# Kernel optimization log

Measured on AMD Instinct MI355X. Metric: run time of the kernel, lower is better.

Reference implementation:

```python
import jax, jax.numpy as jnp
import numpy as np

H = 128

def _gru_cell(x, h, w_ih, w_hh, b_ih, b_hh):
    # PyTorch GRUCell semantics; w_* are [3H, H], gate order r, z, n.
    gi = x @ w_ih.T + b_ih
    gh = h @ w_hh.T + b_hh
    ir, iz, in_ = jnp.split(gi, 3, axis=-1)
    hr, hz, hn = jnp.split(gh, 3, axis=-1)
    r = jax.nn.sigmoid(ir + hr)
    z = jax.nn.sigmoid(iz + hz)
    n = jnp.tanh(in_ + r * hn)
    return (1.0 - z) * n + z * h


def setup_inputs() -> dict:
    key = jax.random.key(0)
    ks = jax.random.split(key, 24)
    s = 0.05
    d = {}
    d["weapon_features"] = jax.random.normal(ks[0], (4, 8, 64, 4), jnp.float32)
    d["target_features"] = jax.random.normal(ks[1], (4, 8, 64, 4), jnp.float32)
    d["edge_features"] = jax.random.uniform(ks[2], (4, 8, 64, 64, 1), jnp.float32)
    # projections (torch Linear convention: weight [out, in])
    d["wp_w"] = jax.random.normal(ks[3], (H, 4), jnp.float32) * s
    d["wp_b"] = jnp.zeros((H,), jnp.float32)
    d["tp_w"] = jax.random.normal(ks[4], (H, 4), jnp.float32) * s
    d["tp_b"] = jnp.zeros((H,), jnp.float32)
    d["ep_w"] = jax.random.normal(ks[5], (H, 1), jnp.float32) * s
    d["ep_b"] = jnp.zeros((H,), jnp.float32)
    # message / edge-update linears [H, 3H]
    d["eu_w"] = jax.random.normal(ks[6], (H, 3 * H), jnp.float32) * s
    d["eu_b"] = jnp.zeros((H,), jnp.float32)
    d["wm_w"] = jax.random.normal(ks[7], (H, 3 * H), jnp.float32) * s
    d["wm_b"] = jnp.zeros((H,), jnp.float32)
    d["tm_w"] = jax.random.normal(ks[8], (H, 3 * H), jnp.float32) * s
    d["tm_b"] = jnp.zeros((H,), jnp.float32)
    # GRU cells
    d["gru_w_ih_w"] = jax.random.normal(ks[9], (3 * H, H), jnp.float32) * s
    d["gru_w_hh_w"] = jax.random.normal(ks[10], (3 * H, H), jnp.float32) * s
    d["gru_b_ih_w"] = jnp.zeros((3 * H,), jnp.float32)
    d["gru_b_hh_w"] = jnp.zeros((3 * H,), jnp.float32)
    d["gru_w_ih_t"] = jax.random.normal(ks[11], (3 * H, H), jnp.float32) * s
    d["gru_w_hh_t"] = jax.random.normal(ks[12], (3 * H, H), jnp.float32) * s
    d["gru_b_ih_t"] = jnp.zeros((3 * H,), jnp.float32)
    d["gru_b_hh_t"] = jnp.zeros((3 * H,), jnp.float32)
    return d


def reference(weapon_features, target_features, edge_features,
              wp_w, wp_b, tp_w, tp_b, ep_w, ep_b,
              eu_w, eu_b, wm_w, wm_b, tm_w, tm_b,
              gru_w_ih_w, gru_w_hh_w, gru_b_ih_w, gru_b_hh_w,
              gru_w_ih_t, gru_w_hh_t, gru_b_ih_t, gru_b_hh_t):
    B, P, W = weapon_features.shape[:3]
    T = target_features.shape[2]
    h = wp_w.shape[0]

    weapon_h = weapon_features @ wp_w.T + wp_b          # [B,P,W,H]
    target_h = target_features @ tp_w.T + tp_b          # [B,P,T,H]
    edge_h = edge_features @ ep_w.T + ep_b              # [B,P,W,T,H]

    # edge_update(cat([w_exp, t_exp, edge_h])) == sum of three slice-linears,
    # broadcast-added; avoids materializing the [B,P,W,T,3H] concat.
    ea, eb, ec = eu_w[:, :h], eu_w[:, h:2 * h], eu_w[:, 2 * h:]
    edge_pre = ((weapon_h @ ea.T)[:, :, :, None, :]
                + (target_h @ eb.T)[:, :, None, :, :]
                + edge_h @ ec.T + eu_b)
    edge_h_new = jnp.tanh(edge_pre)                     # [B,P,W,T,H]

    # weapon_msg(cat([w_exp, t_exp, edge_h_new])).sum(dim=3)
    wa, wb, wc = wm_w[:, :h], wm_w[:, h:2 * h], wm_w[:, 2 * h:]
    weapon_msgs = (T * (weapon_h @ wa.T)
                   + (target_h.sum(axis=2) @ wb.T)[:, :, None, :]
                   + edge_h_new.sum(axis=3) @ wc.T
                   + T * wm_b)                          # [B,P,W,H]

    # target_msg(cat([t_exp, w_exp, edge_h_new])).sum(dim=2)
    ta, tb, tc = tm_w[:, :h], tm_w[:, h:2 * h], tm_w[:, 2 * h:]
    target_msgs = (W * (target_h @ ta.T)
                   + (weapon_h.sum(axis=2) @ tb.T)[:, :, None, :]
                   + edge_h_new.sum(axis=2) @ tc.T
                   + W * tm_b)                          # [B,P,T,H]

    weapon_h_new = _gru_cell(weapon_msgs.reshape(-1, h), weapon_h.reshape(-1, h),
                             gru_w_ih_w, gru_w_hh_w, gru_b_ih_w, gru_b_hh_w)
    weapon_h_new = weapon_h_new.reshape(B, P, W, h)

    target_h_new = _gru_cell(target_msgs.reshape(-1, h), target_h.reshape(-1, h),
                             gru_w_ih_t, gru_w_hh_t, gru_b_ih_t, gru_b_hh_t)
    target_h_new = target_h_new.reshape(B, P, T, h)

    return weapon_h_new, target_h_new, edge_h_new
```

## Files before the change

kernel.cpp:

```cpp
#include <hip/hip_runtime.h>

#define DEV __device__ __forceinline__

constexpr int H  = 128;
constexpr int BP = 32;
constexpr int NR = 2048;

constexpr int WH_OFF    = 0;
constexpr int TH_OFF    = WH_OFF + NR*H;
constexpr int WHS_OFF   = TH_OFF + NR*H;
constexpr int THS_OFF   = WHS_OFF + BP*H;
constexpr int V1_OFF    = THS_OFF + BP*H;
constexpr int C0_OFF    = V1_OFF + H;
constexpr int WT1_OFF   = C0_OFF + H;
constexpr int WT2_OFF   = WT1_OFF + 128*640;
constexpr int WCT_OFF   = WT2_OFF + 128*640;
constexpr int TCT_OFF   = WCT_OFF + 128*128;
constexpr int WIHWT_OFF = TCT_OFF + 128*128;
constexpr int WIHTT_OFF = WIHWT_OFF + 128*384;
constexpr int WBT_OFF   = WIHTT_OFF + 128*384;
constexpr int TBT_OFF   = WBT_OFF + 128*128;
constexpr int OUT1_OFF  = TBT_OFF + 128*128;
constexpr int OUT2_OFF  = OUT1_OFF + NR*640;
constexpr int ESW_OFF   = OUT2_OFF + NR*640;
constexpr int ESTP_OFF  = ESW_OFF + NR*H;
constexpr int MSGW_OFF  = ESTP_OFF + 8*NR*H;
constexpr int MSGT_OFF  = MSGW_OFF + NR*H;
constexpr int GIW_OFF   = MSGT_OFF + NR*H;
constexpr int GIT_OFF   = GIW_OFF + NR*384;
constexpr int WBV_OFF   = GIT_OFF + NR*384;
constexpr int TBV_OFF   = WBV_OFF + BP*H;

DEV float fast_tanh(float x) {
  float e = __builtin_amdgcn_exp2f(x * 2.8853900817779268f);
  return fmaf(-2.0f, __builtin_amdgcn_rcpf(e + 1.0f), 1.0f);
}
DEV float fast_sigmoid(float x) {
  float e = __builtin_amdgcn_exp2f(x * -1.4426950408889634f);
  return __builtin_amdgcn_rcpf(1.0f + e);
}

__global__ __launch_bounds__(256) void k1_proj_transpose(
    const float* __restrict__ wf, const float* __restrict__ tf,
    const float* __restrict__ wp_w, const float* __restrict__ wp_b,
    const float* __restrict__ tp_w, const float* __restrict__ tp_b,
    const float* __restrict__ eu_w, const float* __restrict__ wm_w,
    const float* __restrict__ tm_w,
    const float* __restrict__ whh_w, const float* __restrict__ whh_t,
    const float* __restrict__ wih_w, const float* __restrict__ wih_t,
    float* __restrict__ ws)
{
  int bid = blockIdx.x, tid = threadIdx.x;
  if (bid < 2048) {
    int gid = bid*256 + tid;
    int m = gid >> 7;
    int j = gid & 127;
    int side = m >> 11;
    int n = m & 2047;
    const float* F  = side ? tf : wf;
    const float* Pw = side ? tp_w : wp_w;
    const float* Pb = side ? tp_b : wp_b;
    float4 x  = *(const float4*)&F[n*4];
    float4 wv = *(const float4*)&Pw[j*4];
    float v = x.x*wv.x + x.y*wv.y + x.z*wv.z + x.w*wv.w + Pb[j];
    ws[(side ? TH_OFF : WH_OFF) + n*H + j] = v;
  } else {
    int idx = (bid - 2048)*256 + tid;
    if (idx < 131072) {
      int which = idx >> 14;
      int r = idx & 16383;
      int k = r >> 7, j = r & 127;
      float v; float* dst;
      switch (which) {
        case 0: v = eu_w[j*384 + k];        dst = ws + WT1_OFF + k*640 + j;       break;
        case 1: v = wm_w[j*384 + k];        dst = ws + WT1_OFF + k*640 + 128 + j; break;
        case 2: v = eu_w[j*384 + 128 + k];  dst = ws + WT2_OFF + k*640 + j;       break;
        case 3: v = tm_w[j*384 + k];        dst = ws + WT2_OFF + k*640 + 128 + j; break;
        case 4: v = wm_w[j*384 + 256 + k];  dst = ws + WCT_OFF + k*128 + j;       break;
        case 5: v = tm_w[j*384 + 256 + k];  dst = ws + TCT_OFF + k*128 + j;       break;
        case 6: v = wm_w[j*384 + 128 + k];  dst = ws + WBT_OFF + k*128 + j;       break;
        default:v = tm_w[j*384 + 128 + k];  dst = ws + TBT_OFF + k*128 + j;       break;
      }
      *dst = v;
    } else {
      int idx2 = idx - 131072;
      int which = idx2 / 49152;
      int r = idx2 % 49152;
      int k = r / 384, j = r % 384;
      float v; float* dst;
      switch (which) {
        case 0: v = whh_w[j*128 + k]; dst = ws + WT1_OFF + k*640 + 256 + j; break;
        case 1: v = whh_t[j*128 + k]; dst = ws + WT2_OFF + k*640 + 256 + j; break;
        case 2: v = wih_w[j*128 + k]; dst = ws + WIHWT_OFF + k*384 + j;     break;
        default:v = wih_t[j*128 + k]; dst = ws + WIHTT_OFF + k*384 + j;     break;
      }
      *dst = v;
    }
  }
}

__global__ __launch_bounds__(256) void k2_sums(
    float* __restrict__ ws,
    const float* __restrict__ ep_w, const float* __restrict__ ep_b,
    const float* __restrict__ eu_w, const float* __restrict__ eu_b)
{
  int bid = blockIdx.x, tid = threadIdx.x;
  if (bid < 32) {
    int j = tid & 127, half = tid >> 7;
    const float* src = ws + (half ? TH_OFF : WH_OFF) + bid*64*H + j;
    float s = 0.f;
    #pragma unroll 8
    for (int t = 0; t < 64; ++t) s += src[t*H];
    ws[(half ? THS_OFF : WHS_OFF) + bid*H + j] = s;
  } else if (tid < 128) {
    int j = tid;
    float s1 = 0.f, s0 = 0.f;
    for (int k = 0; k < 128; ++k) {
      float ec = eu_w[j*384 + 256 + k];
      s1 = fmaf(ec, ep_w[k], s1);
      s0 = fmaf(ec, ep_b[k], s0);
    }
    ws[V1_OFF + j] = s1;
    ws[C0_OFF + j] = s0 + eu_b[j];
  }
}

#define FMA4(A, s, Wv) do { A.x = fmaf(s, Wv.x, A.x); A.y = fmaf(s, Wv.y, A.y); \
                            A.z = fmaf(s, Wv.z, A.z); A.w = fmaf(s, Wv.w, A.w); } while (0)

DEV void stage_x_direct(float* Xs, const float* __restrict__ X, int row0, int tid) {
  const float* src = X + row0*128;
  #pragma unroll
  for (int q = 0; q < 4; ++q) {
    int idx = q*1024 + tid*4;
    *(float4*)&Xs[idx] = *(const float4*)&src[idx];
  }
}

DEV void stage_x_sum8(float* Xs, const float* __restrict__ base, int row0, int tid) {
  #pragma unroll
  for (int q = 0; q < 4; ++q) {
    int idx = q*1024 + tid*4;
    float4 s = *(const float4*)&base[row0*128 + idx];
    #pragma unroll
    for (int wt = 1; wt < 8; ++wt) {
      float4 v = *(const float4*)&base[wt*(NR*H) + row0*128 + idx];
      s.x += v.x; s.y += v.y; s.z += v.z; s.w += v.w;
    }
    *(float4*)&Xs[idx] = s;
  }
}

DEV void gemm_core(const float* __restrict__ Wt, int ldw, int j0,
                   const float* Xs, float* Ws, int tid, float4 acc[4])
{
  const int tc = tid & 31, tr = tid >> 5;
  const int jj = tc*4, r0 = tr*4;
  #pragma unroll
  for (int i = 0; i < 4; ++i) acc[i] = make_float4(0.f, 0.f, 0.f, 0.f);
  for (int kc = 0; kc < 128; kc += 32) {
    __syncthreads();
    #pragma unroll
    for (int q = 0; q < 4; ++q) {
      int idx = q*1024 + tid*4;
      int kk = idx >> 7, j = idx & 127;
      *(float4*)&Ws[idx] = *(const float4*)&Wt[(kc+kk)*ldw + j0 + j];
    }
    __syncthreads();
    #pragma unroll
    for (int kk = 0; kk < 32; kk += 4) {
      float4 w0 = *(const float4*)&Ws[(kk+0)*128 + jj];
      float4 w1 = *(const float4*)&Ws[(kk+1)*128 + jj];
      float4 w2 = *(const float4*)&Ws[(kk+2)*128 + jj];
      float4 w3 = *(const float4*)&Ws[(kk+3)*128 + jj];
      #pragma unroll
      for (int rr = 0; rr < 4; ++rr) {
        float4 xq = *(const float4*)&Xs[(r0+rr)*128 + kc + kk];
        FMA4(acc[rr], xq.x, w0);
        FMA4(acc[rr], xq.y, w1);
        FMA4(acc[rr], xq.z, w2);
        FMA4(acc[rr], xq.w, w3);
      }
    }
  }
}

__global__ __launch_bounds__(256) void k3_gemm1(float* __restrict__ ws)
{
  __shared__ float Xs[32*128];
  __shared__ float Wsh[32*128];
  int bid = blockIdx.x, tid = threadIdx.x;
  const int tc = tid & 31, tr = tid >> 5;
  const int jj = tc*4, r0 = tr*4;
  float4 acc[4];
  if (bid < 640) {
    int side = bid >= 320;
    int b2 = bid - (side ? 320 : 0);
    int rt = b2 & 63, ct = b2 >> 6;
    int row0 = rt*32;
    stage_x_direct(Xs, ws + (side ? TH_OFF : WH_OFF), row0, tid);
    gemm_core(ws + (side ? WT2_OFF : WT1_OFF), 640, ct*128, Xs, Wsh, tid, acc);
    float* C = ws + (side ? OUT2_OFF : OUT1_OFF);
    #pragma unroll
    for (int rr = 0; rr < 4; ++rr)
      *(float4*)&C[(row0+r0+rr)*640 + ct*128 + jj] = acc[rr];
  } else {
    int which = bid - 640;
    stage_x_direct(Xs, ws + (which ? WHS_OFF : THS_OFF), 0, tid);
    gemm_core(ws + (which ? TBT_OFF : WBT_OFF), 128, 0, Xs, Wsh, tid, acc);
    float* C = ws + (which ? TBV_OFF : WBV_OFF);
    #pragma unroll
    for (int rr = 0; rr < 4; ++rr)
      *(float4*)&C[(r0+rr)*128 + jj] = acc[rr];
  }
}

__global__ __launch_bounds__(256) void k4_edge(
    const float* __restrict__ ef, float* __restrict__ ws, float* __restrict__ out)
{
  __shared__ float e_lds[8*64];
  __shared__ float red[2][8][128];
  int bid = blockIdx.x, tid = threadIdx.x;
  int bp = bid >> 3, wt = bid & 7;
  int j = tid & 127, tsel = tid >> 7;
  float v1j = ws[V1_OFF + j], c0j = ws[C0_OFF + j];
  {
    const float* esrc = ef + bp*4096 + wt*512;
    *(float2*)&e_lds[tid*2] = *(const float2*)&esrc[tid*2];
  }
  float a_reg[8];
  #pragma unroll
  for (int w = 0; w < 8; ++w)
    a_reg[w] = ws[OUT1_OFF + (bp*64 + wt*8 + w)*640 + j];
  __syncthreads();
  float tsum[8] = {0,0,0,0,0,0,0,0};
  float* edst = out + 524288 + (bp*64 + wt*8)*64*128;
  const float* btp = ws + OUT2_OFF + bp*64*640 + j;
  float* pdst = ws + ESTP_OFF + wt*(NR*H) + bp*64*128 + j;
  for (int i = 0; i < 32; ++i) {
    int t = 2*i + tsel;
    float base = btp[t*640] + c0j;
    float wsum = 0.f;
    #pragma unroll
    for (int w = 0; w < 8; ++w) {
      float ev = e_lds[w*64 + t];
      float pre = a_reg[w] + fmaf(ev, v1j, base);
      float hv = fast_tanh(pre);
      edst[(w*64 + t)*128 + j] = hv;
      tsum[w] += hv;
      wsum += hv;
    }
    pdst[t*128] = wsum;
  }
  #pragma unroll
  for (int w = 0; w < 8; ++w) red[tsel][w][j] = tsum[w];
  __syncthreads();
  if (tsel == 0) {
    #pragma unroll
    for (int w = 0; w < 8; ++w)
      ws[ESW_OFF + (bp*64 + wt*8 + w)*128 + j] = red[0][w][j] + red[1][w][j];
  }
}

__global__ __launch_bounds__(256) void k5_gemm2(
    float* __restrict__ ws, const float* __restrict__ wm_b, const float* __restrict__ tm_b)
{
  __shared__ float Xs[32*128];
  __shared__ float Wsh[32*128];
  int bid = blockIdx.x, tid = threadIdx.x;
  int side = bid >> 6, rt = bid & 63;
  int row0 = rt*32;
  const int tc = tid & 31, tr = tid >> 5;
  const int jj = tc*4, r0 = tr*4;
  if (side == 0) stage_x_direct(Xs, ws + ESW_OFF, row0, tid);
  else           stage_x_sum8(Xs, ws + ESTP_OFF, row0, tid);
  float4 acc[4];
  gemm_core(ws + (side ? TCT_OFF : WCT_OFF), 128, 0, Xs, Wsh, tid, acc);
  const float* OUTx = ws + (side ? OUT2_OFF : OUT1_OFF);
  const float* BV   = ws + (side ? TBV_OFF : WBV_OFF);
  const float* mb   = side ? tm_b : wm_b;
  float* MSG        = ws + (side ? MSGT_OFF : MSGW_OFF);
  float4 b4 = *(const float4*)&mb[jj];
  #pragma unroll
  for (int rr = 0; rr < 4; ++rr) {
    int n = row0 + r0 + rr;
    float4 wa4 = *(const float4*)&OUTx[n*640 + 128 + jj];
    float4 bv4 = *(const float4*)&BV[(n >> 6)*128 + jj];
    float4 r;
    r.x = acc[rr].x + 64.f*wa4.x + bv4.x + 64.f*b4.x;
    r.y = acc[rr].y + 64.f*wa4.y + bv4.y + 64.f*b4.y;
    r.z = acc[rr].z + 64.f*wa4.z + bv4.z + 64.f*b4.z;
    r.w = acc[rr].w + 64.f*wa4.w + bv4.w + 64.f*b4.w;
    *(float4*)&MSG[n*128 + jj] = r;
  }
}

__global__ __launch_bounds__(256) void k6_gemm3(float* __restrict__ ws)
{
  __shared__ float Xs[32*128];
  __shared__ float Wsh[32*128];
  int bid = blockIdx.x, tid = threadIdx.x;
  int side = bid >= 192;
  int b2 = bid - (side ? 192 : 0);
  int rt = b2 & 63, ct = b2 >> 6;
  int row0 = rt*32;
  const int tc = tid & 31, tr = tid >> 5;
  const int jj = tc*4, r0 = tr*4;
  stage_x_direct(Xs, ws + (side ? MSGT_OFF : MSGW_OFF), row0, tid);
  float4 acc[4];
  gemm_core(ws + (side ? WIHTT_OFF : WIHWT_OFF), 384, ct*128, Xs, Wsh, tid, acc);
  float* C = ws + (side ? GIT_OFF : GIW_OFF);
  #pragma unroll
  for (int rr = 0; rr < 4; ++rr)
    *(float4*)&C[(row0+r0+rr)*384 + ct*128 + jj] = acc[rr];
}

__global__ __launch_bounds__(256) void k7_gru(
    const float* __restrict__ ws, float* __restrict__ out,
    const float* __restrict__ bih_w, const float* __restrict__ bhh_w,
    const float* __restrict__ bih_t, const float* __restrict__ bhh_t)
{
  int gid = blockIdx.x*256 + threadIdx.x;
  int m = gid >> 7, j = gid & 127;
  int side = m >> 11, n = m & 2047;
  const float* GI = ws + (side ? GIT_OFF : GIW_OFF) + n*384;
  const float* GH = ws + (side ? OUT2_OFF : OUT1_OFF) + n*640 + 256;
  const float* Hv = ws + (side ? TH_OFF : WH_OFF) + n*128;
  const float* bi = side ? bih_t : bih_w;
  const float* bh = side ? bhh_t : bhh_w;
  float gir = GI[j]       + bi[j];
  float giz = GI[128 + j] + bi[128 + j];
  float gin = GI[256 + j] + bi[256 + j];
  float ghr = GH[j]       + bh[j];
  float ghz = GH[128 + j] + bh[128 + j];
  float ghn = GH[256 + j] + bh[256 + j];
  float r  = fast_sigmoid(gir + ghr);
  float z  = fast_sigmoid(giz + ghz);
  float nn = fast_tanh(gin + r*ghn);
  float h  = Hv[j];
  out[side*262144 + n*128 + j] = (1.f - z)*nn + z*h;
}

extern "C" void kernel_launch(void* const* d_in, const int* in_sizes, int n_in,
                              void* d_out, int out_size, void* d_ws, size_t ws_size,
                              hipStream_t stream)
{
  const float* wf    = (const float*)d_in[0];
  const float* tf    = (const float*)d_in[1];
  const float* ef    = (const float*)d_in[2];
  const float* wp_w  = (const float*)d_in[3];
  const float* wp_b  = (const float*)d_in[4];
  const float* tp_w  = (const float*)d_in[5];
  const float* tp_b  = (const float*)d_in[6];
  const float* ep_w  = (const float*)d_in[7];
  const float* ep_b  = (const float*)d_in[8];
  const float* eu_w  = (const float*)d_in[9];
  const float* eu_b  = (const float*)d_in[10];
  const float* wm_w  = (const float*)d_in[11];
  const float* wm_b  = (const float*)d_in[12];
  const float* tm_w  = (const float*)d_in[13];
  const float* tm_b  = (const float*)d_in[14];
  const float* wih_w = (const float*)d_in[15];
  const float* whh_w = (const float*)d_in[16];
  const float* bih_w = (const float*)d_in[17];
  const float* bhh_w = (const float*)d_in[18];
  const float* wih_t = (const float*)d_in[19];
  const float* whh_t = (const float*)d_in[20];
  const float* bih_t = (const float*)d_in[21];
  const float* bhh_t = (const float*)d_in[22];
  float* ws  = (float*)d_ws;
  float* out = (float*)d_out;

  hipLaunchKernelGGL(k1_proj_transpose, dim3(3328), dim3(256), 0, stream,
                     wf, tf, wp_w, wp_b, tp_w, tp_b, eu_w, wm_w, tm_w,
                     whh_w, whh_t, wih_w, wih_t, ws);
  hipLaunchKernelGGL(k2_sums,  dim3(33),   dim3(256), 0, stream, ws, ep_w, ep_b, eu_w, eu_b);
  hipLaunchKernelGGL(k3_gemm1, dim3(642),  dim3(256), 0, stream, ws);
  hipLaunchKernelGGL(k4_edge,  dim3(256),  dim3(256), 0, stream, ef, ws, out);
  hipLaunchKernelGGL(k5_gemm2, dim3(128),  dim3(256), 0, stream, ws, wm_b, tm_b);
  hipLaunchKernelGGL(k6_gemm3, dim3(384),  dim3(256), 0, stream, ws);
  hipLaunchKernelGGL(k7_gru,   dim3(2048), dim3(256), 0, stream, ws, out,
                     bih_w, bhh_w, bih_t, bhh_t);
}
```

Baseline: 188.7 us.

## Fuse message GEMM, input GEMM and GRU into one kernel; fold sums into projection

Merges the per-node feature sums and edge-projection folding into the first kernel. This works by summing raw 4-wide features and projecting them, rather than summing projected rows in a separate kernel. The edge kernel is split into 512 blocks of 4 weapons each, with the target-side tile staged in LDS. Its partial sums are spread across 16 slices instead of 8. The message GEMM, GRU input GEMM and GRU gate math are fused into one 512-thread kernel on 16-row tiles. This removes three launches and the round trips for the MSG and GI intermediates, at the cost of less per-block data reuse and more partial-sum reads.

```diff
diff --git a/kernel.cpp b/kernel.cpp
--- a/kernel.cpp
+++ b/kernel.cpp
@@ -24,11 +24,7 @@
 constexpr int OUT2_OFF  = OUT1_OFF + NR*640;
 constexpr int ESW_OFF   = OUT2_OFF + NR*640;
 constexpr int ESTP_OFF  = ESW_OFF + NR*H;
-constexpr int MSGW_OFF  = ESTP_OFF + 8*NR*H;
-constexpr int MSGT_OFF  = MSGW_OFF + NR*H;
-constexpr int GIW_OFF   = MSGT_OFF + NR*H;
-constexpr int GIT_OFF   = GIW_OFF + NR*384;
-constexpr int WBV_OFF   = GIT_OFF + NR*384;
+constexpr int WBV_OFF   = ESTP_OFF + 16*NR*H;
 constexpr int TBV_OFF   = WBV_OFF + BP*H;
 
 DEV float fast_tanh(float x) {
@@ -48,8 +44,11 @@
     const float* __restrict__ tm_w,
     const float* __restrict__ whh_w, const float* __restrict__ whh_t,
     const float* __restrict__ wih_w, const float* __restrict__ wih_t,
+    const float* __restrict__ ep_w, const float* __restrict__ ep_b,
+    const float* __restrict__ eu_b,
     float* __restrict__ ws)
 {
+  __shared__ float fs[2][32][4];
   int bid = blockIdx.x, tid = threadIdx.x;
   if (bid < 2048) {
     int gid = bid*256 + tid;
@@ -64,7 +63,7 @@
     float4 wv = *(const float4*)&Pw[j*4];
     float v = x.x*wv.x + x.y*wv.y + x.z*wv.z + x.w*wv.w + Pb[j];
     ws[(side ? TH_OFF : WH_OFF) + n*H + j] = v;
-  } else {
+  } else if (bid < 3328) {
     int idx = (bid - 2048)*256 + tid;
     if (idx < 131072) {
       int which = idx >> 14;
@@ -96,32 +95,41 @@
       }
       *dst = v;
     }
-  }
-}
-
-__global__ __launch_bounds__(256) void k2_sums(
-    float* __restrict__ ws,
-    const float* __restrict__ ep_w, const float* __restrict__ ep_b,
-    const float* __restrict__ eu_w, const float* __restrict__ eu_b)
-{
-  int bid = blockIdx.x, tid = threadIdx.x;
-  if (bid < 32) {
-    int j = tid & 127, half = tid >> 7;
-    const float* src = ws + (half ? TH_OFF : WH_OFF) + bid*64*H + j;
-    float s = 0.f;
-    #pragma unroll 8
-    for (int t = 0; t < 64; ++t) s += src[t*H];
-    ws[(half ? THS_OFF : WHS_OFF) + bid*H + j] = s;
-  } else if (tid < 128) {
-    int j = tid;
-    float s1 = 0.f, s0 = 0.f;
-    for (int k = 0; k < 128; ++k) {
-      float ec = eu_w[j*384 + 256 + k];
-      s1 = fmaf(ec, ep_w[k], s1);
-      s0 = fmaf(ec, ep_b[k], s0);
-    }
-    ws[V1_OFF + j] = s1;
-    ws[C0_OFF + j] = s0 + eu_b[j];
+  } else {
+    {
+      int side = tid >> 7, r = tid & 127;
+      int bp = r >> 2, c = r & 3;
+      const float* F = side ? tf : wf;
+      float s = 0.f;
+      #pragma unroll 8
+      for (int w = 0; w < 64; ++w) s += F[bp*256 + w*4 + c];
+      fs[side][bp][c] = s;
+    }
+    __syncthreads();
+    {
+      int side = tid >> 7, j = tid & 127;
+      const float* Pw = side ? tp_w : wp_w;
+      const float* Pb = side ? tp_b : wp_b;
+      float4 wv = *(const float4*)&Pw[j*4];
+      float pb = Pb[j] * 64.f;
+      float* dst = ws + (side ? THS_OFF : WHS_OFF) + j;
+      #pragma unroll 4
+      for (int bp = 0; bp < 32; ++bp) {
+        float4 f = *(const float4*)&fs[side][bp][0];
+        dst[bp*128] = f.x*wv.x + f.y*wv.y + f.z*wv.z + f.w*wv.w + pb;
+      }
+    }
+    if (tid < 128) {
+      int j = tid;
+      float s1 = 0.f, s0 = 0.f;
+      for (int k = 0; k < 128; ++k) {
+        float ec = eu_w[j*384 + 256 + k];
+        s1 = fmaf(ec, ep_w[k], s1);
+        s0 = fmaf(ec, ep_b[k], s0);
+      }
+      ws[V1_OFF + j] = s1;
+      ws[C0_OFF + j] = s0 + eu_b[j];
+    }
   }
 }
 
@@ -137,34 +145,21 @@
   }
 }
 
-DEV void stage_x_sum8(float* Xs, const float* __restrict__ base, int row0, int tid) {
+template<int RPT, int NTHR>
+DEV void gemm_core2(const float* __restrict__ Wt, int ldw, int j0,
+                    const float* Xs, float* Ws, int tid, float4* acc)
+{
+  const int tc = tid & 31, tr = tid >> 5;
+  const int jj = tc*4, r0 = tr*RPT;
   #pragma unroll
-  for (int q = 0; q < 4; ++q) {
-    int idx = q*1024 + tid*4;
-    float4 s = *(const float4*)&base[row0*128 + idx];
-    #pragma unroll
-    for (int wt = 1; wt < 8; ++wt) {
-      float4 v = *(const float4*)&base[wt*(NR*H) + row0*128 + idx];
-      s.x += v.x; s.y += v.y; s.z += v.z; s.w += v.w;
-    }
-    *(float4*)&Xs[idx] = s;
-  }
-}
-
-DEV void gemm_core(const float* __restrict__ Wt, int ldw, int j0,
-                   const float* Xs, float* Ws, int tid, float4 acc[4])
-{
-  const int tc = tid & 31, tr = tid >> 5;
-  const int jj = tc*4, r0 = tr*4;
-  #pragma unroll
-  for (int i = 0; i < 4; ++i) acc[i] = make_float4(0.f, 0.f, 0.f, 0.f);
+  for (int i = 0; i < RPT; ++i) acc[i] = make_float4(0.f, 0.f, 0.f, 0.f);
   for (int kc = 0; kc < 128; kc += 32) {
     __syncthreads();
     #pragma unroll
-    for (int q = 0; q < 4; ++q) {
-      int idx = q*1024 + tid*4;
-      int kk = idx >> 7, j = idx & 127;
-      *(float4*)&Ws[idx] = *(const float4*)&Wt[(kc+kk)*ldw + j0 + j];
+    for (int q = 0; q < 4096/(NTHR*4); ++q) {
+      int idx = q*(NTHR*4) + tid*4;
+      int kk = idx >> 7, jx = idx & 127;
+      *(float4*)&Ws[idx] = *(const float4*)&Wt[(kc+kk)*ldw + j0 + jx];
     }
     __syncthreads();
     #pragma unroll
@@ -174,7 +169,7 @@
       float4 w2 = *(const float4*)&Ws[(kk+2)*128 + jj];
       float4 w3 = *(const float4*)&Ws[(kk+3)*128 + jj];
       #pragma unroll
-      for (int rr = 0; rr < 4; ++rr) {
+      for (int rr = 0; rr < RPT; ++rr) {
         float4 xq = *(const float4*)&Xs[(r0+rr)*128 + kc + kk];
         FMA4(acc[rr], xq.x, w0);
         FMA4(acc[rr], xq.y, w1);
@@ -199,7 +194,7 @@
     int rt = b2 & 63, ct = b2 >> 6;
     int row0 = rt*32;
     stage_x_direct(Xs, ws + (side ? TH_OFF : WH_OFF), row0, tid);
-    gemm_core(ws + (side ? WT2_OFF : WT1_OFF), 640, ct*128, Xs, Wsh, tid, acc);
+    gemm_core2<4,256>(ws + (side ? WT2_OFF : WT1_OFF), 640, ct*128, Xs, Wsh, tid, acc);
     float* C = ws + (side ? OUT2_OFF : OUT1_OFF);
     #pragma unroll
     for (int rr = 0; rr < 4; ++rr)
@@ -207,7 +202,7 @@
   } else {
     int which = bid - 640;
     stage_x_direct(Xs, ws + (which ? WHS_OFF : THS_OFF), 0, tid);
-    gemm_core(ws + (which ? TBT_OFF : WBT_OFF), 128, 0, Xs, Wsh, tid, acc);
+    gemm_core2<4,256>(ws + (which ? TBT_OFF : WBT_OFF), 128, 0, Xs, Wsh, tid, acc);
     float* C = ws + (which ? TBV_OFF : WBV_OFF);
     #pragma unroll
     for (int rr = 0; rr < 4; ++rr)
@@ -218,127 +213,155 @@
 __global__ __launch_bounds__(256) void k4_edge(
     const float* __restrict__ ef, float* __restrict__ ws, float* __restrict__ out)
 {
-  __shared__ float e_lds[8*64];
-  __shared__ float red[2][8][128];
+  __shared__ float Bs[64*128];
+  __shared__ float e_lds[4*64];
+  __shared__ float red[2][4][128];
   int bid = blockIdx.x, tid = threadIdx.x;
-  int bp = bid >> 3, wt = bid & 7;
+  int bp = bid >> 4, wq = bid & 15;
   int j = tid & 127, tsel = tid >> 7;
   float v1j = ws[V1_OFF + j], c0j = ws[C0_OFF + j];
   {
-    const float* esrc = ef + bp*4096 + wt*512;
-    *(float2*)&e_lds[tid*2] = *(const float2*)&esrc[tid*2];
-  }
-  float a_reg[8];
+    const float* o2 = ws + OUT2_OFF + bp*64*640;
+    #pragma unroll
+    for (int q = 0; q < 8; ++q) {
+      int idx = q*256 + tid;
+      int t = idx >> 5, jq = (idx & 31)*4;
+      *(float4*)&Bs[t*128 + jq] = *(const float4*)&o2[t*640 + jq];
+    }
+  }
+  if (tid < 64) {
+    int w = tid >> 4, t4 = (tid & 15)*4;
+    *(float4*)&e_lds[w*64 + t4] = *(const float4*)&ef[bp*4096 + (wq*4 + w)*64 + t4];
+  }
+  float a_reg[4];
   #pragma unroll
-  for (int w = 0; w < 8; ++w)
-    a_reg[w] = ws[OUT1_OFF + (bp*64 + wt*8 + w)*640 + j];
+  for (int w = 0; w < 4; ++w)
+    a_reg[w] = ws[OUT1_OFF + (bp*64 + wq*4 + w)*640 + j];
   __syncthreads();
-  float tsum[8] = {0,0,0,0,0,0,0,0};
-  float* edst = out + 524288 + (bp*64 + wt*8)*64*128;
-  const float* btp = ws + OUT2_OFF + bp*64*640 + j;
-  float* pdst = ws + ESTP_OFF + wt*(NR*H) + bp*64*128 + j;
+  float tsum[4] = {0.f, 0.f, 0.f, 0.f};
+  float* edst = out + 524288 + (bp*64 + wq*4)*8192 + j;
+  float* pdst = ws + ESTP_OFF + wq*(NR*H) + bp*64*128 + j;
   for (int i = 0; i < 32; ++i) {
     int t = 2*i + tsel;
-    float base = btp[t*640] + c0j;
+    float base = Bs[t*128 + j] + c0j;
     float wsum = 0.f;
     #pragma unroll
-    for (int w = 0; w < 8; ++w) {
+    for (int w = 0; w < 4; ++w) {
       float ev = e_lds[w*64 + t];
       float pre = a_reg[w] + fmaf(ev, v1j, base);
       float hv = fast_tanh(pre);
-      edst[(w*64 + t)*128 + j] = hv;
+      edst[w*8192 + t*128] = hv;
       tsum[w] += hv;
       wsum += hv;
     }
     pdst[t*128] = wsum;
   }
   #pragma unroll
-  for (int w = 0; w < 8; ++w) red[tsel][w][j] = tsum[w];
+  for (int w = 0; w < 4; ++w) red[tsel][w][j] = tsum[w];
   __syncthreads();
   if (tsel == 0) {
     #pragma unroll
-    for (int w = 0; w < 8; ++w)
-      ws[ESW_OFF + (bp*64 + wt*8 + w)*128 + j] = red[0][w][j] + red[1][w][j];
-  }
-}
-
-__global__ __launch_bounds__(256) void k5_gemm2(
-    float* __restrict__ ws, const float* __restrict__ wm_b, const float* __restrict__ tm_b)
-{
-  __shared__ float Xs[32*128];
+    for (int w = 0; w < 4; ++w)
+      ws[ESW_OFF + (bp*64 + wq*4 + w)*128 + j] = red[0][w][j] + red[1][w][j];
+  }
+}
+
+__global__ __launch_bounds__(512) void k5_fused(
+    float* __restrict__ ws, float* __restrict__ out,
+    const float* __restrict__ wm_b, const float* __restrict__ tm_b,
+    const float* __restrict__ bih_w, const float* __restrict__ bhh_w,
+    const float* __restrict__ bih_t, const float* __restrict__ bhh_t)
+{
+  __shared__ float Xs[16*128];
   __shared__ float Wsh[32*128];
   int bid = blockIdx.x, tid = threadIdx.x;
-  int side = bid >> 6, rt = bid & 63;
-  int row0 = rt*32;
+  int side = bid >> 7, rt = bid & 127;
+  int row0 = rt*16;
   const int tc = tid & 31, tr = tid >> 5;
-  const int jj = tc*4, r0 = tr*4;
-  if (side == 0) stage_x_direct(Xs, ws + ESW_OFF, row0, tid);
-  else           stage_x_sum8(Xs, ws + ESTP_OFF, row0, tid);
-  float4 acc[4];
-  gemm_core(ws + (side ? TCT_OFF : WCT_OFF), 128, 0, Xs, Wsh, tid, acc);
-  const float* OUTx = ws + (side ? OUT2_OFF : OUT1_OFF);
-  const float* BV   = ws + (side ? TBV_OFF : WBV_OFF);
-  const float* mb   = side ? tm_b : wm_b;
-  float* MSG        = ws + (side ? MSGT_OFF : MSGW_OFF);
-  float4 b4 = *(const float4*)&mb[jj];
-  #pragma unroll
-  for (int rr = 0; rr < 4; ++rr) {
-    int n = row0 + r0 + rr;
+  const int jj = tc*4;
+  {
+    int r = tid >> 5, jq = (tid & 31)*4;
+    float4 v;
+    if (side == 0) {
+      v = *(const float4*)&ws[ESW_OFF + (row0+r)*128 + jq];
+    } else {
+      v = *(const float4*)&ws[ESTP_OFF + (row0+r)*128 + jq];
+      #pragma unroll
+      for (int p = 1; p < 16; ++p) {
+        float4 u = *(const float4*)&ws[ESTP_OFF + p*(NR*H) + (row0+r)*128 + jq];
+        v.x += u.x; v.y += u.y; v.z += u.z; v.w += u.w;
+      }
+    }
+    *(float4*)&Xs[r*128 + jq] = v;
+  }
+  float4 accm[1];
+  gemm_core2<1,512>(ws + (side ? TCT_OFF : WCT_OFF), 128, 0, Xs, Wsh, tid, accm);
+  __syncthreads();
+  {
+    const float* OUTx = ws + (side ? OUT2_OFF : OUT1_OFF);
+    const float* BV   = ws + (side ? TBV_OFF : WBV_OFF);
+    const float* mb   = side ? tm_b : wm_b;
+    float4 b4 = *(const float4*)&mb[jj];
+    int n = row0 + tr;
     float4 wa4 = *(const float4*)&OUTx[n*640 + 128 + jj];
     float4 bv4 = *(const float4*)&BV[(n >> 6)*128 + jj];
     float4 r;
-    r.x = acc[rr].x + 64.f*wa4.x + bv4.x + 64.f*b4.x;
-    r.y = acc[rr].y + 64.f*wa4.y + bv4.y + 64.f*b4.y;
-    r.z = acc[rr].z + 64.f*wa4.z + bv4.z + 64.f*b4.z;
-    r.w = acc[rr].w + 64.f*wa4.w + bv4.w + 64.f*b4.w;
-    *(float4*)&MSG[n*128 + jj] = r;
-  }
-}
-
-__global__ __launch_bounds__(256) void k6_gemm3(float* __restrict__ ws)
-{
-  __shared__ float Xs[32*128];
-  __shared__ float Wsh[32*128];
-  int bid = blockIdx.x, tid = threadIdx.x;
-  int side = bid >= 192;
-  int b2 = bid - (side ? 192 : 0);
-  int rt = b2 & 63, ct = b2 >> 6;
-  int row0 = rt*32;
-  const int tc = tid & 31, tr = tid >> 5;
-  const int jj = tc*4, r0 = tr*4;
-  stage_x_direct(Xs, ws + (side ? MSGT_OFF : MSGW_OFF), row0, tid);
-  float4 acc[4];
-  gemm_core(ws + (side ? WIHTT_OFF : WIHWT_OFF), 384, ct*128, Xs, Wsh, tid, acc);
-  float* C = ws + (side ? GIT_OFF : GIW_OFF);
-  #pragma unroll
-  for (int rr = 0; rr < 4; ++rr)
-    *(float4*)&C[(row0+r0+rr)*384 + ct*128 + jj] = acc[rr];
-}
-
-__global__ __launch_bounds__(256) void k7_gru(
-    const float* __restrict__ ws, float* __restrict__ out,
-    const float* __restrict__ bih_w, const float* __restrict__ bhh_w,
-    const float* __restrict__ bih_t, const float* __restrict__ bhh_t)
-{
-  int gid = blockIdx.x*256 + threadIdx.x;
-  int m = gid >> 7, j = gid & 127;
-  int side = m >> 11, n = m & 2047;
-  const float* GI = ws + (side ? GIT_OFF : GIW_OFF) + n*384;
-  const float* GH = ws + (side ? OUT2_OFF : OUT1_OFF) + n*640 + 256;
-  const float* Hv = ws + (side ? TH_OFF : WH_OFF) + n*128;
-  const float* bi = side ? bih_t : bih_w;
-  const float* bh = side ? bhh_t : bhh_w;
-  float gir = GI[j]       + bi[j];
-  float giz = GI[128 + j] + bi[128 + j];
-  float gin = GI[256 + j] + bi[256 + j];
-  float ghr = GH[j]       + bh[j];
-  float ghz = GH[128 + j] + bh[128 + j];
-  float ghn = GH[256 + j] + bh[256 + j];
-  float r  = fast_sigmoid(gir + ghr);
-  float z  = fast_sigmoid(giz + ghz);
-  float nn = fast_tanh(gin + r*ghn);
-  float h  = Hv[j];
-  out[side*262144 + n*128 + j] = (1.f - z)*nn + z*h;
+    r.x = accm[0].x + 64.f*(wa4.x + b4.x) + bv4.x;
+    r.y = accm[0].y + 64.f*(wa4.y + b4.y) + bv4.y;
+    r.z = accm[0].z + 64.f*(wa4.z + b4.z) + bv4.z;
+    r.w = accm[0].w + 64.f*(wa4.w + b4.w) + bv4.w;
+    __syncthreads();
+    *(float4*)&Xs[tr*128 + jj] = r;
+  }
+  __syncthreads();
+  const float* WIH = ws + (side ? WIHTT_OFF : WIHWT_OFF);
+  float4 accr[1], accz[1], accn[1];
+  gemm_core2<1,512>(WIH, 384, 0,   Xs, Wsh, tid, accr);
+  gemm_core2<1,512>(WIH, 384, 128, Xs, Wsh, tid, accz);
+  gemm_core2<1,512>(WIH, 384, 256, Xs, Wsh, tid, accn);
+  {
+    const float* OUTx = ws + (side ? OUT2_OFF : OUT1_OFF);
+    const float* Hsrc = ws + (side ? TH_OFF : WH_OFF);
+    const float* bi = side ? bih_t : bih_w;
+    const float* bh = side ? bhh_t : bhh_w;
+    float4 bir = *(const float4*)&bi[jj];
+    float4 biz = *(const float4*)&bi[128 + jj];
+    float4 bin = *(const float4*)&bi[256 + jj];
+    float4 bhr = *(const float4*)&bh[jj];
+    float4 bhz = *(const float4*)&bh[128 + jj];
+    float4 bhn = *(const float4*)&bh[256 + jj];
+    int n = row0 + tr;
+    float4 ghr = *(const float4*)&OUTx[n*640 + 256 + jj];
+    float4 ghz = *(const float4*)&OUTx[n*640 + 384 + jj];
+    float4 ghn = *(const float4*)&OUTx[n*640 + 512 + jj];
+    float4 h4  = *(const float4*)&Hsrc[n*128 + jj];
+    float4 o;
+    {
+      float r = fast_sigmoid(accr[0].x + bir.x + ghr.x + bhr.x);
+      float z = fast_sigmoid(accz[0].x + biz.x + ghz.x + bhz.x);
+      float nn = fast_tanh(accn[0].x + bin.x + r*(ghn.x + bhn.x));
+      o.x = (1.f - z)*nn + z*h4.x;
+    }
+    {
+      float r = fast_sigmoid(accr[0].y + bir.y + ghr.y + bhr.y);
+      float z = fast_sigmoid(accz[0].y + biz.y + ghz.y + bhz.y);
+      float nn = fast_tanh(accn[0].y + bin.y + r*(ghn.y + bhn.y));
+      o.y = (1.f - z)*nn + z*h4.y;
+    }
+    {
+      float r = fast_sigmoid(accr[0].z + bir.z + ghr.z + bhr.z);
+      float z = fast_sigmoid(accz[0].z + biz.z + ghz.z + bhz.z);
+      float nn = fast_tanh(accn[0].z + bin.z + r*(ghn.z + bhn.z));
+      o.z = (1.f - z)*nn + z*h4.z;
+    }
+    {
+      float r = fast_sigmoid(accr[0].w + bir.w + ghr.w + bhr.w);
+      float z = fast_sigmoid(accz[0].w + biz.w + ghz.w + bhz.w);
+      float nn = fast_tanh(accn[0].w + bin.w + r*(ghn.w + bhn.w));
+      o.w = (1.f - z)*nn + z*h4.w;
+    }
+    *(float4*)&out[side*262144 + n*128 + jj] = o;
+  }
 }
 
 extern "C" void kernel_launch(void* const* d_in, const int* in_sizes, int n_in,
@@ -371,14 +394,11 @@
   float* ws  = (float*)d_ws;
   float* out = (float*)d_out;
 
-  hipLaunchKernelGGL(k1_proj_transpose, dim3(3328), dim3(256), 0, stream,
+  hipLaunchKernelGGL(k1_proj_transpose, dim3(3329), dim3(256), 0, stream,
                      wf, tf, wp_w, wp_b, tp_w, tp_b, eu_w, wm_w, tm_w,
-                     whh_w, whh_t, wih_w, wih_t, ws);
-  hipLaunchKernelGGL(k2_sums,  dim3(33),   dim3(256), 0, stream, ws, ep_w, ep_b, eu_w, eu_b);
+                     whh_w, whh_t, wih_w, wih_t, ep_w, ep_b, eu_b, ws);
   hipLaunchKernelGGL(k3_gemm1, dim3(642),  dim3(256), 0, stream, ws);
-  hipLaunchKernelGGL(k4_edge,  dim3(256),  dim3(256), 0, stream, ef, ws, out);
-  hipLaunchKernelGGL(k5_gemm2, dim3(128),  dim3(256), 0, stream, ws, wm_b, tm_b);
-  hipLaunchKernelGGL(k6_gemm3, dim3(384),  dim3(256), 0, stream, ws);
-  hipLaunchKernelGGL(k7_gru,   dim3(2048), dim3(256), 0, stream, ws, out,
-                     bih_w, bhh_w, bih_t, bhh_t);
-}
+  hipLaunchKernelGGL(k4_edge,  dim3(512),  dim3(256), 0, stream, ef, ws, out);
+  hipLaunchKernelGGL(k5_fused, dim3(256),  dim3(512), 0, stream, ws, out,
+                     wm_b, tm_b, bih_w, bhh_w, bih_t, bhh_t);
+}
```

Result: slower. 295.2 us (+56.4%).
